# Kernel optimization log

Measured on AMD Instinct MI355X. Metric: run time of the kernel, lower is better.

The kernel has to match this reference:

```python
import jax, jax.numpy as jnp
import numpy as np
import math

IN_FEATURES = 3072
PADDED = 4096  # next power of two
ACT_BITS = 8
LN_EPS = 1e-6


def hadamard_transform(x):
    """Normalized fast Walsh-Hadamard transform along last dim (power of 2)."""
    n = x.shape[-1]
    m = n.bit_length() - 1  # log2(n)
    shape = x.shape
    y = x.reshape(shape[:-1] + (2,) * m)
    for ax in range(len(shape) - 1, len(shape) - 1 + m):
        a = jnp.take(y, 0, axis=ax)
        b = jnp.take(y, 1, axis=ax)
        y = jnp.stack([a + b, a - b], axis=ax)
    return y.reshape(shape) / jnp.sqrt(jnp.asarray(n, x.dtype))


def activation_quant(x, bits=ACT_BITS):
    """Per-token absmax int-b quant with STE (BitNet style)."""
    qb = 2 ** (bits - 1) - 1  # 127
    scale = qb / jnp.clip(jnp.max(jnp.abs(x), axis=-1, keepdims=True), 1e-5)
    q = jnp.clip(jnp.round(x * scale), -qb - 1, qb) / scale
    return x + jax.lax.stop_gradient(q - x)


def weight_quant(w):
    """Ternary absmean weight quant with STE (as in training path)."""
    scale = jnp.clip(jnp.mean(jnp.abs(w)), 1e-5)
    q = jnp.clip(jnp.round(w / scale), -1.0, 1.0) * scale
    return w + jax.lax.stop_gradient(q - w)


def layer_norm(x, gamma, beta, eps=LN_EPS):
    mu = jnp.mean(x, axis=-1, keepdims=True)
    var = jnp.mean(jnp.square(x - mu), axis=-1, keepdims=True)
    return (x - mu) * jax.lax.rsqrt(var + eps) * gamma + beta


def setup_inputs() -> dict:
    key = jax.random.key(0)
    k1, k2 = jax.random.split(key)
    x = jax.random.normal(k1, (4, 2048, IN_FEATURES), dtype=jnp.float32)
    ln_gamma = jnp.ones((IN_FEATURES,), dtype=jnp.float32)
    ln_beta = jnp.zeros((IN_FEATURES,), dtype=jnp.float32)
    weight = jax.random.normal(k2, (4096, PADDED), dtype=jnp.float32) * 0.02
    return {"x": x, "ln_gamma": ln_gamma, "ln_beta": ln_beta, "weight": weight}


def reference(x, ln_gamma, ln_beta, weight):
    x_norm = layer_norm(x, ln_gamma, ln_beta)
    pad = PADDED - IN_FEATURES
    x_pad = jnp.pad(x_norm, ((0, 0), (0, 0), (0, pad)))
    x_had = hadamard_transform(x_pad)
    x_q = activation_quant(x_had)
    w_q = weight_quant(weight)
    # F.linear: x @ W^T
    out = jnp.einsum('bsd,od->bso', x_q, w_q)
    return out
```

## Files before the change

### kernel.cpp

```cpp
#include <hip/hip_runtime.h>
#include <stdint.h>

#define TOKENS 8192
#define IN_F   3072
#define PAD_F  4096
#define N_OUT  4096
#define K_DIM  4096

using i32x4 = __attribute__((ext_vector_type(4))) int;

#define Q_OFF    0
#define WQ_OFF   33554432
#define AINV_OFF 50331648
#define PART_OFF 50364416
#define WSC_OFF  50380800

__device__ __forceinline__ void gload_lds16(const void* g, void* l) {
    __builtin_amdgcn_global_load_lds(
        (__attribute__((address_space(1))) void*)(void*)g,
        (__attribute__((address_space(3))) void*)l,
        16, 0, 0);
}

__global__ __launch_bounds__(256) void k_wabs(const float* __restrict__ w,
                                              float* __restrict__ partial) {
    int tid = threadIdx.x;
    const float4* w4 = (const float4*)(w + (size_t)blockIdx.x * 4096);
    float s = 0.f;
#pragma unroll
    for (int i = 0; i < 4; ++i) {
        float4 v = w4[tid + i * 256];
        s += fabsf(v.x) + fabsf(v.y) + fabsf(v.z) + fabsf(v.w);
    }
#pragma unroll
    for (int o = 32; o > 0; o >>= 1) s += __shfl_xor(s, o);
    __shared__ float rb[4];
    if ((tid & 63) == 0) rb[tid >> 6] = s;
    __syncthreads();
    if (tid == 0) partial[blockIdx.x] = rb[0] + rb[1] + rb[2] + rb[3];
}

__global__ __launch_bounds__(256) void k_wscale(const float* __restrict__ partial,
                                                float* __restrict__ wsp) {
    int tid = threadIdx.x;
    float s = 0.f;
#pragma unroll
    for (int i = 0; i < 16; ++i) s += partial[tid + i * 256];
#pragma unroll
    for (int o = 32; o > 0; o >>= 1) s += __shfl_xor(s, o);
    __shared__ float rb[4];
    if ((tid & 63) == 0) rb[tid >> 6] = s;
    __syncthreads();
    if (tid == 0)
        wsp[0] = fmaxf((rb[0] + rb[1] + rb[2] + rb[3]) * (1.0f / 16777216.0f), 1e-5f);
}

__global__ __launch_bounds__(256) void k_wquant(const float* __restrict__ w,
                                                const float* __restrict__ wsp,
                                                unsigned int* __restrict__ wq) {
    int idx = blockIdx.x * 256 + threadIdx.x;
    float ws = wsp[0];
    float4 v = ((const float4*)w)[idx];
    int a = (int)rintf(v.x / ws); a = max(-1, min(1, a));
    int b = (int)rintf(v.y / ws); b = max(-1, min(1, b));
    int c = (int)rintf(v.z / ws); c = max(-1, min(1, c));
    int d = (int)rintf(v.w / ws); d = max(-1, min(1, d));
    unsigned int p = (unsigned)(a & 255) | ((unsigned)(b & 255) << 8) |
                     ((unsigned)(c & 255) << 16) | ((unsigned)(d & 255) << 24);
    wq[idx] = p;
}

__global__ __launch_bounds__(256) void k_lnfwht(const float* __restrict__ x,
                                                const float* __restrict__ gamma,
                                                const float* __restrict__ beta,
                                                signed char* __restrict__ q,
                                                float* __restrict__ ainv) {
    __shared__ float s[PAD_F];
    __shared__ float rb[8];
    int tid = threadIdx.x;
    int lane = tid & 63;
    int t = blockIdx.x;
    const float* xr = x + (size_t)t * IN_F;

    float v[16];
    float sum = 0.f;
#pragma unroll
    for (int i = 0; i < 12; ++i) { v[i] = xr[tid + i * 256]; sum += v[i]; }
    v[12] = v[13] = v[14] = v[15] = 0.f;
#pragma unroll
    for (int o = 32; o > 0; o >>= 1) sum += __shfl_xor(sum, o);
    if ((tid & 63) == 0) rb[tid >> 6] = sum;
    __syncthreads();
    float mu = (rb[0] + rb[1] + rb[2] + rb[3]) * (1.0f / 3072.0f);

    float s2 = 0.f;
#pragma unroll
    for (int i = 0; i < 12; ++i) { float d = v[i] - mu; s2 += d * d; }
#pragma unroll
    for (int o = 32; o > 0; o >>= 1) s2 += __shfl_xor(s2, o);
    if ((tid & 63) == 0) rb[4 + (tid >> 6)] = s2;
    __syncthreads();
    float var = (rb[4] + rb[5] + rb[6] + rb[7]) * (1.0f / 3072.0f);
    float rstd = 1.0f / sqrtf(var + 1e-6f);

#pragma unroll
    for (int i = 0; i < 12; ++i)
        v[i] = (v[i] - mu) * rstd * gamma[tid + i * 256] + beta[tid + i * 256];

#pragma unroll
    for (int b = 1; b < 16; b <<= 1) {
#pragma unroll
        for (int i = 0; i < 16; ++i) {
            if (!(i & b)) {
                float a0 = v[i], b0 = v[i | b];
                v[i] = a0 + b0;
                v[i | b] = a0 - b0;
            }
        }
    }
#pragma unroll
    for (int m = 1; m <= 32; m <<= 1) {
#pragma unroll
        for (int i = 0; i < 16; ++i) {
            float p = __shfl_xor(v[i], m);
            v[i] = (lane & m) ? (p - v[i]) : (v[i] + p);
        }
    }
#pragma unroll
    for (int m = 64; m <= 128; m <<= 1) {
        __syncthreads();
#pragma unroll
        for (int i = 0; i < 16; ++i) s[tid + i * 256] = v[i];
        __syncthreads();
#pragma unroll
        for (int i = 0; i < 16; ++i) {
            float p = s[(tid ^ m) + i * 256];
            v[i] = (tid & m) ? (p - v[i]) : (v[i] + p);
        }
    }

    float mx = 0.f;
#pragma unroll
    for (int i = 0; i < 16; ++i) mx = fmaxf(mx, fabsf(v[i]));
#pragma unroll
    for (int o = 32; o > 0; o >>= 1) mx = fmaxf(mx, __shfl_xor(mx, o));
    __syncthreads();
    if ((tid & 63) == 0) rb[tid >> 6] = mx;
    __syncthreads();
    float amraw = fmaxf(fmaxf(rb[0], rb[1]), fmaxf(rb[2], rb[3]));
    float amax = fmaxf(amraw * (1.0f / 64.0f), 1e-5f);
    float scale = 127.0f / amax;
    if (tid == 0) ainv[t] = amax * (1.0f / 127.0f);

    signed char* qr = q + (size_t)t * PAD_F;
#pragma unroll
    for (int i = 0; i < 16; ++i) {
        int qi = (int)rintf(v[i] * (1.0f / 64.0f) * scale);
        qi = max(-128, min(127, qi));
        qr[tid + i * 256] = (signed char)qi;
    }
}

#define BK 64
#define NT (K_DIM / BK)

#define VMW(n) asm volatile("s_waitcnt vmcnt(" #n ")" ::: "memory")

__global__ __launch_bounds__(512, 2) void k_gemm(const signed char* __restrict__ Aq,
                                                 const signed char* __restrict__ Wq,
                                                 const float* __restrict__ ainv,
                                                 const float* __restrict__ wsp,
                                                 float* __restrict__ out) {
    __shared__ signed char sA[4][128 * 128];
    __shared__ signed char sB[4][128 * 128];

    int tid = threadIdx.x;
    int lane = tid & 63, wid = tid >> 6;

    int bid = blockIdx.x;
    int xcd = bid & 7, li = bid >> 3;
    int bmb = xcd * 4 + (li & 3);
    int bnb = li >> 2;
    size_t bm0 = (size_t)bmb * 256, bn0 = (size_t)bnb * 256;

    int wm = wid >> 2, wn = wid & 3;

    int rr = lane >> 3, pp = lane & 7;
    int Lg = pp ^ rr;
    int spar = Lg >> 2, sh = Lg & 3;
    const signed char* gA = Aq + (bm0 + (size_t)(wid * 32 + 2 * rr + spar)) * K_DIM + sh * 16;
    const signed char* gB = Wq + (bn0 + (size_t)(wid * 32 + 2 * rr + spar)) * K_DIM + sh * 16;

    int fr = lane & 15, hh = lane >> 4;
    int pos = (((fr & 1) << 2) | hh) ^ (fr >> 1);
    int abase = (wm * 64 + (fr >> 1)) * 8 + pos;
    int bbase = (wn * 32 + (fr >> 1)) * 8 + pos;

    i32x4 acc[8][4];
#pragma unroll
    for (int m = 0; m < 8; ++m)
#pragma unroll
        for (int n = 0; n < 4; ++n) acc[m][n] = (i32x4){0, 0, 0, 0};

    i32x4 afA[8], bfA[4], afB[8], bfB[4];

    auto STAGE = [&](int b, int t) {
        size_t k0 = (size_t)t * BK;
        gload_lds16(gA + k0, &sA[b][(wid * 16) * 128]);
        gload_lds16(gA + k0 + (size_t)16 * K_DIM, &sA[b][(wid * 16 + 8) * 128]);
        gload_lds16(gB + k0, &sB[b][(wid * 16) * 128]);
        gload_lds16(gB + k0 + (size_t)16 * K_DIM, &sB[b][(wid * 16 + 8) * 128]);
    };

#define LOADF(B, AF, BF) do {                                           \
    const i32x4* va = (const i32x4*)&sA[B][0];                          \
    const i32x4* vb = (const i32x4*)&sB[B][0];                          \
    _Pragma("unroll")                                                   \
    for (int mf = 0; mf < 8; ++mf) AF[mf] = va[abase + mf * 64];        \
    _Pragma("unroll")                                                   \
    for (int nf = 0; nf < 4; ++nf) BF[nf] = vb[bbase + nf * 64];        \
} while (0)

#define COMPUTE(AF, BF) do {                                            \
    __builtin_amdgcn_s_setprio(1);                                      \
    _Pragma("unroll")                                                   \
    for (int mf = 0; mf < 8; ++mf)                                      \
        _Pragma("unroll")                                               \
        for (int nf = 0; nf < 4; ++nf)                                  \
            acc[mf][nf] = __builtin_amdgcn_mfma_i32_16x16x64_i8(        \
                AF[mf], BF[nf], acc[mf][nf], 0, 0, 0);                  \
    __builtin_amdgcn_s_setprio(0);                                      \
} while (0)

#define BODY(T, AFC, BFC, AFN, BFN) do {                                \
    STAGE((T + 3) & 3, T + 3);                                          \
    VMW(8);                                                             \
    __builtin_amdgcn_sched_barrier(0);                                  \
    __builtin_amdgcn_s_barrier();                                       \
    __builtin_amdgcn_sched_barrier(0);                                  \
    LOADF((T + 1) & 3, AFN, BFN);                                       \
    COMPUTE(AFC, BFC);                                                  \
    asm volatile("s_waitcnt lgkmcnt(0)" ::: "memory");                  \
    __builtin_amdgcn_sched_barrier(0);                                  \
} while (0)

    STAGE(0, 0);
    STAGE(1, 1);
    STAGE(2, 2);
    VMW(8);
    __builtin_amdgcn_sched_barrier(0);
    __builtin_amdgcn_s_barrier();
    __builtin_amdgcn_sched_barrier(0);
    LOADF(0, afA, bfA);
    asm volatile("s_waitcnt lgkmcnt(0)" ::: "memory");
    __builtin_amdgcn_sched_barrier(0);

#pragma unroll 1
    for (int t = 0; t < NT - 4; t += 2) {
        BODY(t, afA, bfA, afB, bfB);
        BODY(t + 1, afB, bfB, afA, bfA);
    }
    BODY(NT - 4, afA, bfA, afB, bfB);
    VMW(4);
    __builtin_amdgcn_sched_barrier(0);
    __builtin_amdgcn_s_barrier();
    __builtin_amdgcn_sched_barrier(0);
    LOADF(2, afA, bfA);
    COMPUTE(afB, bfB);
    asm volatile("s_waitcnt lgkmcnt(0)" ::: "memory");
    __builtin_amdgcn_sched_barrier(0);
    VMW(0);
    __builtin_amdgcn_sched_barrier(0);
    __builtin_amdgcn_s_barrier();
    __builtin_amdgcn_sched_barrier(0);
    LOADF(3, afB, bfB);
    COMPUTE(afA, bfA);
    asm volatile("s_waitcnt lgkmcnt(0)" ::: "memory");
    __builtin_amdgcn_sched_barrier(0);
    COMPUTE(afB, bfB);

    float wsc = wsp[0];
#pragma unroll
    for (int mf = 0; mf < 8; ++mf) {
        size_t row0 = bm0 + wm * 128 + mf * 16 + hh * 4;
#pragma unroll
        for (int r = 0; r < 4; ++r) {
            size_t row = row0 + r;
            float sa = wsc * ainv[row];
#pragma unroll
            for (int nf = 0; nf < 4; ++nf) {
                size_t col = bn0 + wn * 64 + nf * 16 + fr;
                out[row * N_OUT + col] = (float)acc[mf][nf][r] * sa;
            }
        }
    }
#undef LOADF
#undef COMPUTE
#undef BODY
}

extern "C" void kernel_launch(void* const* d_in, const int* in_sizes, int n_in,
                              void* d_out, int out_size, void* d_ws, size_t ws_size,
                              hipStream_t stream) {
    const float* x     = (const float*)d_in[0];
    const float* gamma = (const float*)d_in[1];
    const float* beta  = (const float*)d_in[2];
    const float* w     = (const float*)d_in[3];
    float* out = (float*)d_out;
    char* ws = (char*)d_ws;

    signed char* q   = (signed char*)(ws + Q_OFF);
    signed char* wq  = (signed char*)(ws + WQ_OFF);
    float* ainv      = (float*)(ws + AINV_OFF);
    float* partial   = (float*)(ws + PART_OFF);
    float* wsp       = (float*)(ws + WSC_OFF);

    k_wabs<<<dim3(4096), dim3(256), 0, stream>>>(w, partial);
    k_wscale<<<dim3(1), dim3(256), 0, stream>>>(partial, wsp);
    k_wquant<<<dim3(16384), dim3(256), 0, stream>>>(w, wsp, (unsigned int*)wq);
    k_lnfwht<<<dim3(TOKENS), dim3(256), 0, stream>>>(x, gamma, beta, q, ainv);
    k_gemm<<<dim3(512), dim3(512), 0, stream>>>(q, wq, ainv, wsp, out);
}
```

Before: 213.4 us.

## Fuse weight-abs reduction into LN/FWHT kernel and switch GEMM to 32x32x32 MFMA

The weight absmax partial sums now run as extra blocks of the LayerNorm+Hadamard kernel and combine through a 64-bit fixed-point atomic, which removes two kernel launches and the single-block scale kernel. The GEMM inner loop moves from 16x16x64 i8 MFMA to 32x32x32 i8 MFMA with a new fragment layout and epilogue mapping, which means fewer MFMA issues and fewer LDS fragment reads per tile. Costs include a memset launch, atomic contention on one address, and fixed-point rounding in the weight scale.

```diff
diff --git a/kernel.cpp b/kernel.cpp
--- a/kernel.cpp
+++ b/kernel.cpp
@@ -7,13 +7,15 @@
 #define N_OUT  4096
 #define K_DIM  4096
 
-using i32x4 = __attribute__((ext_vector_type(4))) int;
+using i32x4  = __attribute__((ext_vector_type(4))) int;
+using i32x16 = __attribute__((ext_vector_type(16))) int;
 
 #define Q_OFF    0
 #define WQ_OFF   33554432
 #define AINV_OFF 50331648
-#define PART_OFF 50364416
-#define WSC_OFF  50380800
+#define WTOT_OFF 50364416
+
+#define WTOT_TO_SCALE (1.0 / (67108864.0 * 16777216.0))
 
 __device__ __forceinline__ void gload_lds16(const void* g, void* l) {
     __builtin_amdgcn_global_load_lds(
@@ -22,44 +24,125 @@
         16, 0, 0);
 }
 
-__global__ __launch_bounds__(256) void k_wabs(const float* __restrict__ w,
-                                              float* __restrict__ partial) {
+__global__ __launch_bounds__(256) void k_fused1(const float* __restrict__ x,
+                                                const float* __restrict__ gamma,
+                                                const float* __restrict__ beta,
+                                                const float* __restrict__ w,
+                                                signed char* __restrict__ q,
+                                                float* __restrict__ ainv,
+                                                unsigned long long* __restrict__ wtot) {
+    __shared__ float s[PAD_F];
+    __shared__ float rb[8];
     int tid = threadIdx.x;
-    const float4* w4 = (const float4*)(w + (size_t)blockIdx.x * 4096);
-    float s = 0.f;
-#pragma unroll
-    for (int i = 0; i < 4; ++i) {
-        float4 v = w4[tid + i * 256];
-        s += fabsf(v.x) + fabsf(v.y) + fabsf(v.z) + fabsf(v.w);
-    }
-#pragma unroll
-    for (int o = 32; o > 0; o >>= 1) s += __shfl_xor(s, o);
-    __shared__ float rb[4];
-    if ((tid & 63) == 0) rb[tid >> 6] = s;
+    int lane = tid & 63;
+    int bid = blockIdx.x;
+
+    if (bid >= TOKENS) {
+        const float4* w4 = (const float4*)(w + (size_t)(bid - TOKENS) * 4096);
+        float sm = 0.f;
+#pragma unroll
+        for (int i = 0; i < 4; ++i) {
+            float4 v = w4[tid + i * 256];
+            sm += fabsf(v.x) + fabsf(v.y) + fabsf(v.z) + fabsf(v.w);
+        }
+#pragma unroll
+        for (int o = 32; o > 0; o >>= 1) sm += __shfl_xor(sm, o);
+        if ((tid & 63) == 0) rb[tid >> 6] = sm;
+        __syncthreads();
+        if (tid == 0) {
+            float bs = rb[0] + rb[1] + rb[2] + rb[3];
+            atomicAdd(wtot, (unsigned long long)(bs * 67108864.0f));
+        }
+        return;
+    }
+
+    int t = bid;
+    const float* xr = x + (size_t)t * IN_F;
+
+    float v[16];
+    float sum = 0.f;
+#pragma unroll
+    for (int i = 0; i < 12; ++i) { v[i] = xr[tid + i * 256]; sum += v[i]; }
+    v[12] = v[13] = v[14] = v[15] = 0.f;
+#pragma unroll
+    for (int o = 32; o > 0; o >>= 1) sum += __shfl_xor(sum, o);
+    if ((tid & 63) == 0) rb[tid >> 6] = sum;
     __syncthreads();
-    if (tid == 0) partial[blockIdx.x] = rb[0] + rb[1] + rb[2] + rb[3];
-}
-
-__global__ __launch_bounds__(256) void k_wscale(const float* __restrict__ partial,
-                                                float* __restrict__ wsp) {
-    int tid = threadIdx.x;
-    float s = 0.f;
-#pragma unroll
-    for (int i = 0; i < 16; ++i) s += partial[tid + i * 256];
-#pragma unroll
-    for (int o = 32; o > 0; o >>= 1) s += __shfl_xor(s, o);
-    __shared__ float rb[4];
-    if ((tid & 63) == 0) rb[tid >> 6] = s;
+    float mu = (rb[0] + rb[1] + rb[2] + rb[3]) * (1.0f / 3072.0f);
+
+    float s2 = 0.f;
+#pragma unroll
+    for (int i = 0; i < 12; ++i) { float d = v[i] - mu; s2 += d * d; }
+#pragma unroll
+    for (int o = 32; o > 0; o >>= 1) s2 += __shfl_xor(s2, o);
+    if ((tid & 63) == 0) rb[4 + (tid >> 6)] = s2;
     __syncthreads();
-    if (tid == 0)
-        wsp[0] = fmaxf((rb[0] + rb[1] + rb[2] + rb[3]) * (1.0f / 16777216.0f), 1e-5f);
+    float var = (rb[4] + rb[5] + rb[6] + rb[7]) * (1.0f / 3072.0f);
+    float rstd = 1.0f / sqrtf(var + 1e-6f);
+
+#pragma unroll
+    for (int i = 0; i < 12; ++i)
+        v[i] = (v[i] - mu) * rstd * gamma[tid + i * 256] + beta[tid + i * 256];
+
+#pragma unroll
+    for (int b = 1; b < 16; b <<= 1) {
+#pragma unroll
+        for (int i = 0; i < 16; ++i) {
+            if (!(i & b)) {
+                float a0 = v[i], b0 = v[i | b];
+                v[i] = a0 + b0;
+                v[i | b] = a0 - b0;
+            }
+        }
+    }
+#pragma unroll
+    for (int m = 1; m <= 32; m <<= 1) {
+#pragma unroll
+        for (int i = 0; i < 16; ++i) {
+            float p = __shfl_xor(v[i], m);
+            v[i] = (lane & m) ? (p - v[i]) : (v[i] + p);
+        }
+    }
+#pragma unroll
+    for (int m = 64; m <= 128; m <<= 1) {
+        __syncthreads();
+#pragma unroll
+        for (int i = 0; i < 16; ++i) s[tid + i * 256] = v[i];
+        __syncthreads();
+#pragma unroll
+        for (int i = 0; i < 16; ++i) {
+            float p = s[(tid ^ m) + i * 256];
+            v[i] = (tid & m) ? (p - v[i]) : (v[i] + p);
+        }
+    }
+
+    float mx = 0.f;
+#pragma unroll
+    for (int i = 0; i < 16; ++i) mx = fmaxf(mx, fabsf(v[i]));
+#pragma unroll
+    for (int o = 32; o > 0; o >>= 1) mx = fmaxf(mx, __shfl_xor(mx, o));
+    __syncthreads();
+    if ((tid & 63) == 0) rb[tid >> 6] = mx;
+    __syncthreads();
+    float amraw = fmaxf(fmaxf(rb[0], rb[1]), fmaxf(rb[2], rb[3]));
+    float amax = fmaxf(amraw * (1.0f / 64.0f), 1e-5f);
+    float scale = 127.0f / amax;
+    if (tid == 0) ainv[t] = amax * (1.0f / 127.0f);
+
+    signed char* qr = q + (size_t)t * PAD_F;
+#pragma unroll
+    for (int i = 0; i < 16; ++i) {
+        int qi = (int)rintf(v[i] * (1.0f / 64.0f) * scale);
+        qi = max(-128, min(127, qi));
+        qr[tid + i * 256] = (signed char)qi;
+    }
 }
 
 __global__ __launch_bounds__(256) void k_wquant(const float* __restrict__ w,
-                                                const float* __restrict__ wsp,
+                                                const unsigned long long* __restrict__ wtot,
                                                 unsigned int* __restrict__ wq) {
     int idx = blockIdx.x * 256 + threadIdx.x;
-    float ws = wsp[0];
+    float ws = (float)fmax((double)(*wtot) * WTOT_TO_SCALE, 1e-5);
     float4 v = ((const float4*)w)[idx];
     int a = (int)rintf(v.x / ws); a = max(-1, min(1, a));
     int b = (int)rintf(v.y / ws); b = max(-1, min(1, b));
@@ -70,106 +153,16 @@
     wq[idx] = p;
 }
 
-__global__ __launch_bounds__(256) void k_lnfwht(const float* __restrict__ x,
-                                                const float* __restrict__ gamma,
-                                                const float* __restrict__ beta,
-                                                signed char* __restrict__ q,
-                                                float* __restrict__ ainv) {
-    __shared__ float s[PAD_F];
-    __shared__ float rb[8];
-    int tid = threadIdx.x;
-    int lane = tid & 63;
-    int t = blockIdx.x;
-    const float* xr = x + (size_t)t * IN_F;
-
-    float v[16];
-    float sum = 0.f;
-#pragma unroll
-    for (int i = 0; i < 12; ++i) { v[i] = xr[tid + i * 256]; sum += v[i]; }
-    v[12] = v[13] = v[14] = v[15] = 0.f;
-#pragma unroll
-    for (int o = 32; o > 0; o >>= 1) sum += __shfl_xor(sum, o);
-    if ((tid & 63) == 0) rb[tid >> 6] = sum;
-    __syncthreads();
-    float mu = (rb[0] + rb[1] + rb[2] + rb[3]) * (1.0f / 3072.0f);
-
-    float s2 = 0.f;
-#pragma unroll
-    for (int i = 0; i < 12; ++i) { float d = v[i] - mu; s2 += d * d; }
-#pragma unroll
-    for (int o = 32; o > 0; o >>= 1) s2 += __shfl_xor(s2, o);
-    if ((tid & 63) == 0) rb[4 + (tid >> 6)] = s2;
-    __syncthreads();
-    float var = (rb[4] + rb[5] + rb[6] + rb[7]) * (1.0f / 3072.0f);
-    float rstd = 1.0f / sqrtf(var + 1e-6f);
-
-#pragma unroll
-    for (int i = 0; i < 12; ++i)
-        v[i] = (v[i] - mu) * rstd * gamma[tid + i * 256] + beta[tid + i * 256];
-
-#pragma unroll
-    for (int b = 1; b < 16; b <<= 1) {
-#pragma unroll
-        for (int i = 0; i < 16; ++i) {
-            if (!(i & b)) {
-                float a0 = v[i], b0 = v[i | b];
-                v[i] = a0 + b0;
-                v[i | b] = a0 - b0;
-            }
-        }
-    }
-#pragma unroll
-    for (int m = 1; m <= 32; m <<= 1) {
-#pragma unroll
-        for (int i = 0; i < 16; ++i) {
-            float p = __shfl_xor(v[i], m);
-            v[i] = (lane & m) ? (p - v[i]) : (v[i] + p);
-        }
-    }
-#pragma unroll
-    for (int m = 64; m <= 128; m <<= 1) {
-        __syncthreads();
-#pragma unroll
-        for (int i = 0; i < 16; ++i) s[tid + i * 256] = v[i];
-        __syncthreads();
-#pragma unroll
-        for (int i = 0; i < 16; ++i) {
-            float p = s[(tid ^ m) + i * 256];
-            v[i] = (tid & m) ? (p - v[i]) : (v[i] + p);
-        }
-    }
-
-    float mx = 0.f;
-#pragma unroll
-    for (int i = 0; i < 16; ++i) mx = fmaxf(mx, fabsf(v[i]));
-#pragma unroll
-    for (int o = 32; o > 0; o >>= 1) mx = fmaxf(mx, __shfl_xor(mx, o));
-    __syncthreads();
-    if ((tid & 63) == 0) rb[tid >> 6] = mx;
-    __syncthreads();
-    float amraw = fmaxf(fmaxf(rb[0], rb[1]), fmaxf(rb[2], rb[3]));
-    float amax = fmaxf(amraw * (1.0f / 64.0f), 1e-5f);
-    float scale = 127.0f / amax;
-    if (tid == 0) ainv[t] = amax * (1.0f / 127.0f);
-
-    signed char* qr = q + (size_t)t * PAD_F;
-#pragma unroll
-    for (int i = 0; i < 16; ++i) {
-        int qi = (int)rintf(v[i] * (1.0f / 64.0f) * scale);
-        qi = max(-128, min(127, qi));
-        qr[tid + i * 256] = (signed char)qi;
-    }
-}
-
 #define BK 64
 #define NT (K_DIM / BK)
 
 #define VMW(n) asm volatile("s_waitcnt vmcnt(" #n ")" ::: "memory")
+#define SB0()  __builtin_amdgcn_sched_barrier(0)
 
 __global__ __launch_bounds__(512, 2) void k_gemm(const signed char* __restrict__ Aq,
                                                  const signed char* __restrict__ Wq,
                                                  const float* __restrict__ ainv,
-                                                 const float* __restrict__ wsp,
+                                                 const unsigned long long* __restrict__ wtot,
                                                  float* __restrict__ out) {
     __shared__ signed char sA[4][128 * 128];
     __shared__ signed char sB[4][128 * 128];
@@ -191,18 +184,21 @@
     const signed char* gA = Aq + (bm0 + (size_t)(wid * 32 + 2 * rr + spar)) * K_DIM + sh * 16;
     const signed char* gB = Wq + (bn0 + (size_t)(wid * 32 + 2 * rr + spar)) * K_DIM + sh * 16;
 
-    int fr = lane & 15, hh = lane >> 4;
-    int pos = (((fr & 1) << 2) | hh) ^ (fr >> 1);
-    int abase = (wm * 64 + (fr >> 1)) * 8 + pos;
-    int bbase = (wn * 32 + (fr >> 1)) * 8 + pos;
-
-    i32x4 acc[8][4];
-#pragma unroll
-    for (int m = 0; m < 8; ++m)
-#pragma unroll
-        for (int n = 0; n < 4; ++n) acc[m][n] = (i32x4){0, 0, 0, 0};
-
-    i32x4 afA[8], bfA[4], afB[8], bfB[4];
+    int r32 = lane & 31, ks = lane >> 5;
+    int q7 = (r32 >> 1) & 7;
+    int pq = ((r32 & 1) << 2) | ks;
+    int pos0 = pq ^ q7;
+    int pos1 = (pq | 2) ^ q7;
+    int abase = (wm * 64 + (r32 >> 1)) * 8;
+    int bbase = (wn * 32 + (r32 >> 1)) * 8;
+
+    i32x16 acc[4][2];
+#pragma unroll
+    for (int m = 0; m < 4; ++m)
+#pragma unroll
+        for (int n = 0; n < 2; ++n) acc[m][n] = (i32x16)(0);
+
+    i32x4 afA[2][4], bfA[2][2], afB[2][4], bfB[2][2];
 
     auto STAGE = [&](int b, int t) {
         size_t k0 = (size_t)t * BK;
@@ -212,48 +208,56 @@
         gload_lds16(gB + k0 + (size_t)16 * K_DIM, &sB[b][(wid * 16 + 8) * 128]);
     };
 
-#define LOADF(B, AF, BF) do {                                           \
-    const i32x4* va = (const i32x4*)&sA[B][0];                          \
-    const i32x4* vb = (const i32x4*)&sB[B][0];                          \
+#define LOADF(Bb, AF, BF) do {                                          \
+    const i32x4* va = (const i32x4*)&sA[Bb][0];                         \
+    const i32x4* vb = (const i32x4*)&sB[Bb][0];                         \
     _Pragma("unroll")                                                   \
-    for (int mf = 0; mf < 8; ++mf) AF[mf] = va[abase + mf * 64];        \
+    for (int mf = 0; mf < 4; ++mf) {                                    \
+        AF[0][mf] = va[abase + mf * 128 + pos0];                        \
+        AF[1][mf] = va[abase + mf * 128 + pos1];                        \
+    }                                                                   \
     _Pragma("unroll")                                                   \
-    for (int nf = 0; nf < 4; ++nf) BF[nf] = vb[bbase + nf * 64];        \
+    for (int nf = 0; nf < 2; ++nf) {                                    \
+        BF[0][nf] = vb[bbase + nf * 128 + pos0];                        \
+        BF[1][nf] = vb[bbase + nf * 128 + pos1];                        \
+    }                                                                   \
 } while (0)
 
 #define COMPUTE(AF, BF) do {                                            \
     __builtin_amdgcn_s_setprio(1);                                      \
     _Pragma("unroll")                                                   \
-    for (int mf = 0; mf < 8; ++mf)                                      \
+    for (int kk = 0; kk < 2; ++kk)                                      \
         _Pragma("unroll")                                               \
-        for (int nf = 0; nf < 4; ++nf)                                  \
-            acc[mf][nf] = __builtin_amdgcn_mfma_i32_16x16x64_i8(        \
-                AF[mf], BF[nf], acc[mf][nf], 0, 0, 0);                  \
+        for (int mf = 0; mf < 4; ++mf)                                  \
+            _Pragma("unroll")                                           \
+            for (int nf = 0; nf < 2; ++nf)                              \
+                acc[mf][nf] = __builtin_amdgcn_mfma_i32_32x32x32_i8(    \
+                    AF[kk][mf], BF[kk][nf], acc[mf][nf], 0, 0, 0);      \
     __builtin_amdgcn_s_setprio(0);                                      \
 } while (0)
 
 #define BODY(T, AFC, BFC, AFN, BFN) do {                                \
     STAGE((T + 3) & 3, T + 3);                                          \
     VMW(8);                                                             \
-    __builtin_amdgcn_sched_barrier(0);                                  \
+    SB0();                                                              \
     __builtin_amdgcn_s_barrier();                                       \
-    __builtin_amdgcn_sched_barrier(0);                                  \
+    SB0();                                                              \
     LOADF((T + 1) & 3, AFN, BFN);                                       \
     COMPUTE(AFC, BFC);                                                  \
     asm volatile("s_waitcnt lgkmcnt(0)" ::: "memory");                  \
-    __builtin_amdgcn_sched_barrier(0);                                  \
+    SB0();                                                              \
 } while (0)
 
     STAGE(0, 0);
     STAGE(1, 1);
     STAGE(2, 2);
     VMW(8);
-    __builtin_amdgcn_sched_barrier(0);
+    SB0();
     __builtin_amdgcn_s_barrier();
-    __builtin_amdgcn_sched_barrier(0);
+    SB0();
     LOADF(0, afA, bfA);
     asm volatile("s_waitcnt lgkmcnt(0)" ::: "memory");
-    __builtin_amdgcn_sched_barrier(0);
+    SB0();
 
 #pragma unroll 1
     for (int t = 0; t < NT - 4; t += 2) {
@@ -262,35 +266,36 @@
     }
     BODY(NT - 4, afA, bfA, afB, bfB);
     VMW(4);
-    __builtin_amdgcn_sched_barrier(0);
+    SB0();
     __builtin_amdgcn_s_barrier();
-    __builtin_amdgcn_sched_barrier(0);
+    SB0();
     LOADF(2, afA, bfA);
     COMPUTE(afB, bfB);
     asm volatile("s_waitcnt lgkmcnt(0)" ::: "memory");
-    __builtin_amdgcn_sched_barrier(0);
+    SB0();
     VMW(0);
-    __builtin_amdgcn_sched_barrier(0);
+    SB0();
     __builtin_amdgcn_s_barrier();
-    __builtin_amdgcn_sched_barrier(0);
+    SB0();
     LOADF(3, afB, bfB);
     COMPUTE(afA, bfA);
     asm volatile("s_waitcnt lgkmcnt(0)" ::: "memory");
-    __builtin_amdgcn_sched_barrier(0);
+    SB0();
     COMPUTE(afB, bfB);
 
-    float wsc = wsp[0];
-#pragma unroll
-    for (int mf = 0; mf < 8; ++mf) {
-        size_t row0 = bm0 + wm * 128 + mf * 16 + hh * 4;
-#pragma unroll
-        for (int r = 0; r < 4; ++r) {
-            size_t row = row0 + r;
+    float wsc = (float)fmax((double)(*wtot) * WTOT_TO_SCALE, 1e-5);
+    int c31 = lane & 31, hi2 = lane >> 5;
+#pragma unroll
+    for (int mf = 0; mf < 4; ++mf) {
+        size_t rowb = bm0 + wm * 128 + mf * 32 + 4 * hi2;
+#pragma unroll
+        for (int reg = 0; reg < 16; ++reg) {
+            size_t row = rowb + (reg & 3) + 8 * (reg >> 2);
             float sa = wsc * ainv[row];
 #pragma unroll
-            for (int nf = 0; nf < 4; ++nf) {
-                size_t col = bn0 + wn * 64 + nf * 16 + fr;
-                out[row * N_OUT + col] = (float)acc[mf][nf][r] * sa;
+            for (int nf = 0; nf < 2; ++nf) {
+                size_t col = bn0 + wn * 64 + nf * 32 + c31;
+                out[row * N_OUT + col] = (float)acc[mf][nf][reg] * sa;
             }
         }
     }
@@ -312,12 +317,10 @@
     signed char* q   = (signed char*)(ws + Q_OFF);
     signed char* wq  = (signed char*)(ws + WQ_OFF);
     float* ainv      = (float*)(ws + AINV_OFF);
-    float* partial   = (float*)(ws + PART_OFF);
-    float* wsp       = (float*)(ws + WSC_OFF);
-
-    k_wabs<<<dim3(4096), dim3(256), 0, stream>>>(w, partial);
-    k_wscale<<<dim3(1), dim3(256), 0, stream>>>(partial, wsp);
-    k_wquant<<<dim3(16384), dim3(256), 0, stream>>>(w, wsp, (unsigned int*)wq);
-    k_lnfwht<<<dim3(TOKENS), dim3(256), 0, stream>>>(x, gamma, beta, q, ainv);
-    k_gemm<<<dim3(512), dim3(512), 0, stream>>>(q, wq, ainv, wsp, out);
-}
+    unsigned long long* wtot = (unsigned long long*)(ws + WTOT_OFF);
+
+    hipMemsetAsync((void*)wtot, 0, 8, stream);
+    k_fused1<<<dim3(TOKENS + 4096), dim3(256), 0, stream>>>(x, gamma, beta, w, q, ainv, wtot);
+    k_wquant<<<dim3(16384), dim3(256), 0, stream>>>(w, wtot, (unsigned int*)wq);
+    k_gemm<<<dim3(512), dim3(512), 0, stream>>>(q, wq, ainv, wtot, out);
+}
```

Measured after the change: 263.2 us. 1.23x slower.
